# Performance work log

Hardware: AMD Instinct MI355X
Metric: run time of the kernel (lower is better)

The kernel has to match this reference:

```python
import jax, jax.numpy as jnp
import numpy as np

D = 256; H = 4; DK = D // H
MAX_ATOMS = 13; EDGE_NUM = 78; PAD = 799; K = 20
PREFIX = MAX_ATOMS * 2 + 2 + EDGE_NUM * 4   # 340, tokens that get positional encoding
SEQ = PREFIX + K                             # 360
NPAIR = EDGE_NUM + MAX_ATOMS                 # 91 atom pairs (i,j), j up to max_atoms
DFF = 2048; MSP = 800; B = 256

# ---- static pair / gather index tables (numpy, computed once) ----
def _pairs():
    pi, pj, pe = [], [], []
    for i in range(MAX_ATOMS):
        base = sum(MAX_ATOMS - jj - 1 for jj in range(i))  # getEdgeIdx prefix
        for j in range(i + 1, MAX_ATOMS + 1):
            pi.append(i); pj.append(j); pe.append(base + (j - i) - 1)
    return np.array(pi), np.array(pj), np.array(pe)

PI, PJ, PEI = _pairs()
_eb = MAX_ATOMS * 2 + 2 + 2 * PEI           # edge feature start in encoder output (stride 2)
GIDX = np.stack([2*PI, 2*PI+1, 2*PJ, 2*PJ+1, _eb, _eb+1, _eb+2, _eb+3], axis=1)  # (91,8)
ZMASK = np.ones((NPAIR, 8), np.float32)
ZMASK[PJ == MAX_ATOMS, 4:] = 0.0            # j == max_atoms -> edge slots zeroed
ES = (MAX_ATOMS + 1) * 2 + 4 * PEI          # edge slice start in raw src (stride 4)
EIDX = ES[:, None] + np.arange(4)[None, :]  # (91,4)

def _pe_table():
    pe = np.zeros((PREFIX, D), np.float32)
    pos = np.arange(PREFIX, dtype=np.float64)[:, None]
    ev = np.arange(0, D, 2)
    pe[:, ev] = np.sin(pos / 10000.0 ** (2 * ev / D))
    pe[:, ev + 1] = np.cos(pos / 10000.0 ** (2 * (ev + 1) / D))
    return jnp.asarray(pe)

PETAB = _pe_table()

def _norm(x, a, b):
    mu = x.mean(-1, keepdims=True)
    sd = x.std(-1, keepdims=True, ddof=1)   # torch std is unbiased
    return a * (x - mu) / (sd + 1e-6) + b

def _out_mask(src):
    # vectorized get_pad_mask10; later conditions override earlier ones
    ai = src[:, 2*PI + 1]; aj = src[:, 2*PJ + 1]
    ti = src[:, 2*PI];     tj = src[:, 2*PJ]
    c1 = (ai == 2) | (aj == 2)                                  # -> [0,0,1]
    c2 = (tj == 1) | (ai == 1) | (aj == 1)                      # -> [0,1,1]
    c3 = (ti == PAD) | (tj == PAD) | (ai == 0) | (aj == 0)      # -> [1,1,1]
    c4 = jnp.asarray(PJ < MAX_ATOMS)[None, :] & jnp.any(src[:, EIDX] == 1, axis=-1)
    m111 = c3 | c4
    return jnp.stack([m111, m111 | c2, m111 | c2 | c1], axis=-1)  # (B,91,3) bool


def setup_inputs() -> dict:
    key = jax.random.key(0)
    ks = jax.random.split(key, 12)
    g = lambda k, shape, s=0.02: jax.random.normal(k, shape, jnp.float32) * s
    emb = g(ks[0], (MSP, D), 1.0).at[PAD].set(0.0)  # nn.Embedding zeroes padding row
    return {
        'src': jax.random.randint(ks[1], (B, SEQ), 0, MSP, dtype=jnp.int32),
        'emb': emb,
        'wq': g(ks[2], (D, D)), 'bq': jnp.zeros((D,), jnp.float32),
        'wk': g(ks[3], (D, D)), 'bk': jnp.zeros((D,), jnp.float32),
        'wv': g(ks[4], (D, D)), 'bv': jnp.zeros((D,), jnp.float32),
        'wo': g(ks[5], (D, D)), 'bo': jnp.zeros((D,), jnp.float32),
        'n1a': jnp.ones((D,), jnp.float32), 'n1b': jnp.zeros((D,), jnp.float32),
        'n2a': jnp.ones((D,), jnp.float32), 'n2b': jnp.zeros((D,), jnp.float32),
        'w1': g(ks[6], (D, DFF)), 'b1': jnp.zeros((DFF,), jnp.float32),
        'w2': g(ks[7], (DFF, D)), 'b2': jnp.zeros((D,), jnp.float32),
        'wl': g(ks[8], (8 * D, 3)), 'bl': jnp.zeros((3,), jnp.float32),
    }


def reference(src, emb, wq, bq, wk, bk, wv, bv, wo, bo, n1a, n1b, n2a, n2b,
              w1, b1, w2, b2, wl, bl):
    Bn, S = src.shape
    x = emb[src]                                             # (B,S,D)
    # positional encoding (scale + PE) only on first PREFIX tokens, dropout=eval/no-op
    xp = x[:, :PREFIX] * jnp.sqrt(jnp.float32(D)) + PETAB
    x = jnp.concatenate([xp, x[:, PREFIX:]], axis=1)
    pad = src != PAD                                         # (B,S) query-row mask
    # encoder layer (pre-norm, residual)
    x2 = _norm(x, n1a, n1b)
    def heads(w, b):
        return (x2 @ w + b).reshape(Bn, S, H, DK).transpose(0, 2, 1, 3)
    q, kk, v = heads(wq, bq), heads(wk, bk), heads(wv, bv)
    sc = jnp.einsum('bhqd,bhkd->bhqk', q, kk) / jnp.sqrt(jnp.float32(DK))
    sc = jnp.where(pad[:, None, :, None], sc, jnp.float32(-1e9))  # mask broadcasts over keys
    ctx = jnp.einsum('bhqk,bhkd->bhqd', jax.nn.softmax(sc, axis=-1), v)
    x = x + ctx.transpose(0, 2, 1, 3).reshape(Bn, S, D) @ wo + bo
    x2 = _norm(x, n2a, n2b)
    x = x + jax.nn.relu(x2 @ w1 + b1) @ w2 + b2
    # triangular atom-pair gather + concat, vectorized via static index table
    feat = x[:, GIDX] * jnp.asarray(ZMASK)[None, :, :, None]  # (B,91,8,D)
    logits = feat.reshape(Bn, NPAIR, 8 * D) @ wl + bl         # (B,91,3)
    return jnp.where(_out_mask(src), jnp.float32(-1e9), logits)
```

## Files before the change

kernel.cpp:

```cpp
#include <hip/hip_runtime.h>
#include <hip/hip_bf16.h>
#include <math.h>


using bf16 = __hip_bfloat16;
typedef __attribute__((ext_vector_type(4))) float f32x4;
typedef __attribute__((ext_vector_type(16))) float f32x16;
typedef long long i64;
typedef unsigned char uchar;

static __device__ __forceinline__ float wave_sum64(float v){
  #pragma unroll
  for (int o = 32; o >= 1; o >>= 1) v += __shfl_xor(v, o, 64);
  return v;
}

static __device__ __forceinline__ void gl_lds16(const void* g, void* l){
  __builtin_amdgcn_global_load_lds((const __attribute__((address_space(1))) void*)g,
                                   (__attribute__((address_space(3))) void*)l, 16, 0, 0);
}

static __device__ __forceinline__ void barrier_lgkm(){
  asm volatile("s_waitcnt lgkmcnt(0)" ::: "memory");
  __builtin_amdgcn_s_barrier();
}

static __device__ __forceinline__ unsigned pack2(float a, float b){
  union { bf16 h[2]; unsigned u; } u;
  u.h[0] = __float2bfloat16(a); u.h[1] = __float2bfloat16(b);
  return u.u;
}

static __device__ __forceinline__ uchar f2f8(float v){
  return (uchar)(__builtin_amdgcn_cvt_pk_fp8_f32(v, 0.f, 0, false) & 0xff);
}
static __device__ __forceinline__ unsigned pack4_fp8(float a, float b, float c, float d){
  int v = __builtin_amdgcn_cvt_pk_fp8_f32(a, b, 0, false);
  v = __builtin_amdgcn_cvt_pk_fp8_f32(c, d, v, true);
  return (unsigned)v;
}

static __device__ __forceinline__ float fexp2(float x){
  float r;
  asm("v_exp_f32 %0, %1" : "=v"(r) : "v"(x));
  return r;
}

__global__ __launch_bounds__(256) void cvt_all(
    const float* s0, const float* s1, const float* s2, const float* s3,
    const float* s4, const float* s5,
    uchar* d0, uchar* d1, uchar* d2, uchar* d3, uchar* d4, uchar* d5)
{
  __shared__ float t[32][33];
  const float* srcs[6] = {s0, s1, s2, s3, s4, s5};
  uchar* dsts[6] = {d0, d1, d2, d3, d4, d5};
  const int Ks[6] = {256, 256, 256, 256, 256, 2048};
  const int Ns[6] = {256, 256, 256, 256, 2048, 256};
  const int offs[7] = {0, 64, 128, 192, 256, 768, 1280};
  int bid = blockIdx.x, j = 5;
  #pragma unroll
  for (int q = 4; q >= 0; q--) if (bid < offs[q + 1]) j = q;
  int local = bid - offs[j];
  int K = Ks[j], N = Ns[j];
  const float* src = srcs[j];
  uchar* dst = dsts[j];
  int kt = K >> 5;
  int kb = (local % kt) * 32, nb = (local / kt) * 32;
  int tx = threadIdx.x & 31, ty = threadIdx.x >> 5;
  #pragma unroll
  for (int dy = 0; dy < 32; dy += 8)
    t[ty + dy][tx] = src[(size_t)(kb + ty + dy) * N + nb + tx];
  __syncthreads();
  #pragma unroll
  for (int dy = 0; dy < 32; dy += 8)
    dst[(size_t)(nb + ty + dy) * K + kb + tx] = f2f8(t[tx][ty + dy]);
}

__global__ __launch_bounds__(256) void embed_ln1(
    const int* __restrict__ src, const float* __restrict__ emb,
    const float* __restrict__ na, const float* __restrict__ nb,
    bf16* __restrict__ x, uchar* __restrict__ xn8)
{
  int row  = blockIdx.x * 4 + (threadIdx.x >> 6);
  int lane = threadIdx.x & 63;
  int s = row % 360;
  int tok = src[row];
  float4 v = *(const float4*)(emb + (size_t)tok * 256 + lane * 4);
  float vv[4] = {v.x, v.y, v.z, v.w};
  if (s < 340){
    const float C = (-2.0f / 256.0f) * 13.287712379549449f;
    #pragma unroll
    for (int t = 0; t < 4; t++){
      int c = lane * 4 + t;
      float ang = (float)s * exp2f(C * (float)c);
      float pe = (c & 1) ? cosf(ang) : sinf(ang);
      vv[t] = 16.0f * vv[t] + pe;
    }
  }
  float sum = wave_sum64(vv[0] + vv[1] + vv[2] + vv[3]);
  float mu = sum * (1.0f / 256.0f);
  float d0 = vv[0]-mu, d1 = vv[1]-mu, d2 = vv[2]-mu, d3 = vv[3]-mu;
  float sq = wave_sum64(d0*d0 + d1*d1 + d2*d2 + d3*d3);
  float inv = 1.0f / (sqrtf(sq * (1.0f / 255.0f)) + 1e-6f);
  bf16 xo[4] = { __float2bfloat16(vv[0]), __float2bfloat16(vv[1]),
                 __float2bfloat16(vv[2]), __float2bfloat16(vv[3]) };
  *(uint2*)(x + (size_t)row * 256 + lane * 4) = *(uint2*)xo;
  float4 a4 = *(const float4*)(na + lane * 4);
  float4 b4 = *(const float4*)(nb + lane * 4);
  unsigned u = pack4_fp8(a4.x * d0 * inv + b4.x, a4.y * d1 * inv + b4.y,
                         a4.z * d2 * inv + b4.z, a4.w * d3 * inv + b4.w);
  *(unsigned*)(xn8 + (size_t)row * 256 + lane * 4) = u;
}

__global__ __launch_bounds__(256) void ln_k8(
    const bf16* __restrict__ x, const float* __restrict__ na,
    const float* __restrict__ nb, uchar* __restrict__ xn8)
{
  int row  = blockIdx.x * 4 + (threadIdx.x >> 6);
  int lane = threadIdx.x & 63;
  uint2 raw = *(const uint2*)(x + (size_t)row * 256 + lane * 4);
  bf16* xr = (bf16*)&raw;
  float v0 = __bfloat162float(xr[0]), v1 = __bfloat162float(xr[1]);
  float v2 = __bfloat162float(xr[2]), v3 = __bfloat162float(xr[3]);
  float sum = wave_sum64(v0 + v1 + v2 + v3);
  float mu = sum * (1.0f / 256.0f);
  float d0 = v0-mu, d1 = v1-mu, d2 = v2-mu, d3 = v3-mu;
  float sq = wave_sum64(d0*d0 + d1*d1 + d2*d2 + d3*d3);
  float inv = 1.0f / (sqrtf(sq * (1.0f / 255.0f)) + 1e-6f);
  float4 a4 = *(const float4*)(na + lane * 4);
  float4 b4 = *(const float4*)(nb + lane * 4);
  unsigned u = pack4_fp8(a4.x * d0 * inv + b4.x, a4.y * d1 * inv + b4.y,
                         a4.z * d2 * inv + b4.z, a4.w * d3 * inv + b4.w);
  *(unsigned*)(xn8 + (size_t)row * 256 + lane * 4) = u;
}

template<int MODE>
__global__ __launch_bounds__(256) void gemm_k256(
    const uchar* __restrict__ A, const uchar* __restrict__ Bt,
    const float* __restrict__ bias,
    uchar* __restrict__ out8, bf16* __restrict__ xres,
    int N, int nTiles,
    const float* __restrict__ bq, const float* __restrict__ bk)
{
  __shared__ __align__(16) char smem[65536];
  uchar* As = (uchar*)smem;
  uchar* Bs = (uchar*)(smem + 32768);
  uchar* S8 = (uchar*)smem;
  bf16 (*Cs)[136] = (bf16 (*)[136])smem;
  int chunk = gridDim.x >> 3;
  int bi = (blockIdx.x & 7) * chunk + (blockIdx.x >> 3);
  int m0 = (bi / nTiles) * 128, n0 = (bi % nTiles) * 128;
  int tid = threadIdx.x;
  int wave = tid >> 6, lane = tid & 63;
  int wm = (wave >> 1) * 64, wn = (wave & 1) * 64;
  int r32 = lane & 31, half = lane >> 5;

  #pragma unroll
  for (int j = 0; j < 8; j++){
    int c = j * 256 + tid;
    int row = c >> 4, p = c & 15;
    int sl = (p & 8) | ((p & 7) ^ (row & 7));
    gl_lds16(A  + (size_t)(m0 + row) * 256 + sl * 16, As + (size_t)c * 16);
    gl_lds16(Bt + (size_t)(n0 + row) * 256 + sl * 16, Bs + (size_t)c * 16);
  }

  f32x16 acc[2][2];
  #pragma unroll
  for (int mb = 0; mb < 2; mb++)
    #pragma unroll
    for (int nb = 0; nb < 2; nb++)
      #pragma unroll
      for (int e = 0; e < 16; e++) acc[mb][nb][e] = 0.f;

  __syncthreads();

  #pragma unroll
  for (int c = 0; c < 8; c++){
    int l0 = 2 * c + half;
    i64 alo[2], ahi[2], blo[2], bhi[2];
    #pragma unroll
    for (int mb = 0; mb < 2; mb++){
      int row = wm + mb * 32 + r32;
      int st = (l0 & 8) | ((l0 & 7) ^ (row & 7));
      uint4 v = *(const uint4*)(As + row * 256 + st * 16);
      alo[mb] = *(const i64*)&v.x;  ahi[mb] = *(const i64*)&v.z;
    }
    #pragma unroll
    for (int nb = 0; nb < 2; nb++){
      int row = wn + nb * 32 + r32;
      int st = (l0 & 8) | ((l0 & 7) ^ (row & 7));
      uint4 v = *(const uint4*)(Bs + row * 256 + st * 16);
      blo[nb] = *(const i64*)&v.x;  bhi[nb] = *(const i64*)&v.z;
    }
    #pragma unroll
    for (int mb = 0; mb < 2; mb++)
      #pragma unroll
      for (int nb = 0; nb < 2; nb++){
        if (MODE == 5){
          acc[mb][nb] = __builtin_amdgcn_mfma_f32_32x32x16_fp8_fp8(alo[mb], blo[nb], acc[mb][nb], 0, 0, 0);
          acc[mb][nb] = __builtin_amdgcn_mfma_f32_32x32x16_fp8_fp8(ahi[mb], bhi[nb], acc[mb][nb], 0, 0, 0);
        } else {
          acc[mb][nb] = __builtin_amdgcn_mfma_f32_32x32x16_fp8_fp8(blo[nb], alo[mb], acc[mb][nb], 0, 0, 0);
          acc[mb][nb] = __builtin_amdgcn_mfma_f32_32x32x16_fp8_fp8(bhi[nb], ahi[mb], acc[mb][nb], 0, 0, 0);
        }
      }
  }

  __syncthreads();

  if (MODE == 4){
    const int region = n0 >> 8;
    const float* bb = (region == 0 ? bq : bk);
    #pragma unroll
    for (int mb = 0; mb < 2; mb++){
      int m_l = wm + mb * 32 + r32;
      #pragma unroll
      for (int nb = 0; nb < 2; nb++)
        #pragma unroll
        for (int g = 0; g < 4; g++){
          int n_l = wn + nb * 32 + g * 8 + half * 4;
          int bidx = (n0 & 255) + n_l;
          float v0 = acc[mb][nb][g * 4 + 0] + bb[bidx + 0];
          float v1 = acc[mb][nb][g * 4 + 1] + bb[bidx + 1];
          float v2 = acc[mb][nb][g * 4 + 2] + bb[bidx + 2];
          float v3 = acc[mb][nb][g * 4 + 3] + bb[bidx + 3];
          *(unsigned*)(S8 + m_l * 136 + n_l) = pack4_fp8(v0, v1, v2, v3);
        }
    }
    __syncthreads();
    int lr = tid >> 1, seg = tid & 1;
    #pragma unroll
    for (int j = 0; j < 4; j++){
      int nl = seg * 64 + j * 16;
      uint2 a = *(uint2*)(S8 + lr * 136 + nl);
      uint2 b = *(uint2*)(S8 + lr * 136 + nl + 8);
      uint4 st = make_uint4(a.x, a.y, b.x, b.y);
      int m = m0 + lr;
      int b_ = m / 360, s = m - b_ * 360;
      int nnl = (n0 & 255) + nl;
      int h = nnl >> 6, dk = nnl & 63;
      size_t roff = (region == 1) ? 23592960ull : 0ull;
      *(uint4*)(out8 + roff + ((size_t)(b_ * 4 + h) * 360 + s) * 64 + dk) = st;
    }
  } else if (MODE == 5){
    #pragma unroll
    for (int nb = 0; nb < 2; nb++){
      int n_l = wn + nb * 32 + r32;
      float bv_ = bias[n0 + n_l];
      #pragma unroll
      for (int mb = 0; mb < 2; mb++)
        #pragma unroll
        for (int g = 0; g < 4; g++){
          int m_l = wm + mb * 32 + g * 8 + half * 4;
          *(unsigned*)(S8 + n_l * 136 + m_l) =
              pack4_fp8(acc[mb][nb][g * 4 + 0] + bv_, acc[mb][nb][g * 4 + 1] + bv_,
                        acc[mb][nb][g * 4 + 2] + bv_, acc[mb][nb][g * 4 + 3] + bv_);
        }
    }
    __syncthreads();
    int nn = tid >> 1, part = tid & 1;
    int nnl = n0 + nn;
    int h = nnl >> 6, dk = nnl & 63;
    #pragma unroll
    for (int j0 = 0; j0 < 64; j0 += 8){
      int mm = m0 + part * 64 + j0;
      int b_ = mm / 360, s = mm - b_ * 360;
      uint2 val = *(uint2*)(S8 + nn * 136 + part * 64 + j0);
      *(uint2*)(out8 + ((size_t)((b_ * 4 + h) * 64 + dk)) * 360 + s) = val;
    }
  } else {
    #pragma unroll
    for (int hb = 0; hb < 2; hb++){
      if ((wave >> 1) == hb){
        #pragma unroll
        for (int mb = 0; mb < 2; mb++){
          int ml = mb * 32 + r32;
          #pragma unroll
          for (int nb = 0; nb < 2; nb++)
            #pragma unroll
            for (int g = 0; g < 4; g++){
              int nl0 = wn + nb * 32 + g * 8 + half * 4;
              float v0 = acc[mb][nb][g * 4 + 0] + bias[n0 + nl0 + 0];
              float v1 = acc[mb][nb][g * 4 + 1] + bias[n0 + nl0 + 1];
              float v2 = acc[mb][nb][g * 4 + 2] + bias[n0 + nl0 + 2];
              float v3 = acc[mb][nb][g * 4 + 3] + bias[n0 + nl0 + 3];
              *(unsigned*)(&Cs[ml][nl0])     = pack2(v0, v1);
              *(unsigned*)(&Cs[ml][nl0 + 2]) = pack2(v2, v3);
            }
        }
      }
      __syncthreads();
      int mbase = m0 + hb * 64;
      int lr = tid >> 2, seg = tid & 3;
      bf16* op = xres + (size_t)(mbase + lr) * 256 + n0 + seg * 32;
      #pragma unroll
      for (int j = 0; j < 4; j++){
        uint4 cv = *(uint4*)(&Cs[lr][seg * 32 + j * 8]);
        uint4 xv = *(uint4*)(op + j * 8);
        bf16* ca = (bf16*)&cv; bf16* xa = (bf16*)&xv;
        bf16 o8[8];
        #pragma unroll
        for (int t = 0; t < 8; t++)
          o8[t] = __float2bfloat16(__bfloat162float(ca[t]) + __bfloat162float(xa[t]));
        *(uint4*)(op + j * 8) = *(uint4*)o8;
      }
      __syncthreads();
    }
  }
}

__global__ __launch_bounds__(512) void gemm_ffn(
    const uchar* __restrict__ A, const uchar* __restrict__ W1t,
    const uchar* __restrict__ W2t, const float* __restrict__ b1,
    const float* __restrict__ b2, bf16* __restrict__ xres)
{
  extern __shared__ __align__(16) char sm[];
  const int W1OFF = 32768, W2OFF = 98304;
  int bi = (blockIdx.x & 7) * 90 + (blockIdx.x >> 3);
  int m0 = bi * 128;
  int tid = threadIdx.x;
  int wave = tid >> 6, lane = tid & 63;
  int wm = (wave & 1) * 64, wn = (wave >> 1) * 64;
  int wnh = (wave >> 1) * 32;
  int r32 = lane & 31, half = lane >> 5;

  #pragma unroll
  for (int j = 0; j < 4; j++){
    int c = j * 512 + tid;
    int row = c >> 4, p = c & 15;
    int sl = (p & 8) | ((p & 7) ^ (row & 7));
    gl_lds16(A + (size_t)(m0 + row) * 256 + sl * 16, sm + c * 16);
  }
  #pragma unroll
  for (int j = 0; j < 4; j++){
    int c = j * 512 + tid;
    int row1 = c >> 4, p1 = c & 15;
    int sl1 = (p1 & 8) | ((p1 & 7) ^ (row1 & 7));
    gl_lds16(W1t + (size_t)row1 * 256 + sl1 * 16, sm + W1OFF + c * 16);
    int row2 = c >> 3, p2 = c & 7;
    int sl2 = p2 ^ (row2 & 7);
    gl_lds16(W2t + (size_t)row2 * 2048 + sl2 * 16, sm + W2OFF + c * 16);
  }

  f32x16 acc2[2][2];
  #pragma unroll
  for (int mb = 0; mb < 2; mb++)
    #pragma unroll
    for (int nb = 0; nb < 2; nb++)
      #pragma unroll
      for (int e = 0; e < 16; e++) acc2[mb][nb][e] = 0.f;

  __syncthreads();

  i64 Alo[2][8], Ahi[2][8];
  #pragma unroll
  for (int c = 0; c < 8; c++){
    int l0 = 2 * c + half;
    #pragma unroll
    for (int mb = 0; mb < 2; mb++){
      int row = wm + mb * 32 + r32;
      int st = (l0 & 8) | ((l0 & 7) ^ (row & 7));
      uint4 v = *(const uint4*)(sm + row * 256 + st * 16);
      Alo[mb][c] = *(const i64*)&v.x;  Ahi[mb][c] = *(const i64*)&v.z;
    }
  }

  int cur = 0;
  for (int s = 0; s < 16; s++){
    const int w1o = W1OFF + cur * 32768;
    const int w2o = W2OFF + cur * 32768;

    f32x16 acc1[2];
    #pragma unroll
    for (int mb = 0; mb < 2; mb++)
      #pragma unroll
      for (int e = 0; e < 16; e++) acc1[mb][e] = 0.f;
    #pragma unroll
    for (int c = 0; c < 8; c++){
      int l0 = 2 * c + half;
      int roww = wnh + r32;
      int stw = (l0 & 8) | ((l0 & 7) ^ (roww & 7));
      uint4 w = *(const uint4*)(sm + w1o + roww * 256 + stw * 16);
      i64 wlo = *(const i64*)&w.x, whi = *(const i64*)&w.z;
      #pragma unroll
      for (int mb = 0; mb < 2; mb++){
        acc1[mb] = __builtin_amdgcn_mfma_f32_32x32x16_fp8_fp8(wlo, Alo[mb][c], acc1[mb], 0, 0, 0);
        acc1[mb] = __builtin_amdgcn_mfma_f32_32x32x16_fp8_fp8(whi, Ahi[mb][c], acc1[mb], 0, 0, 0);
      }
    }
    barrier_lgkm();

    if (s < 15){
      int nxt = cur ^ 1;
      #pragma unroll
      for (int j = 0; j < 4; j++){
        int c = j * 512 + tid;
        int row1 = c >> 4, p1 = c & 15;
        int sl1 = (p1 & 8) | ((p1 & 7) ^ (row1 & 7));
        gl_lds16(W1t + (size_t)((s + 1) * 128 + row1) * 256 + sl1 * 16,
                 sm + W1OFF + nxt * 32768 + c * 16);
        int row2 = c >> 3, p2 = c & 7;
        int sl2 = p2 ^ (row2 & 7);
        gl_lds16(W2t + (size_t)row2 * 2048 + (s + 1) * 128 + sl2 * 16,
                 sm + W2OFF + nxt * 32768 + c * 16);
      }
    }

    #pragma unroll
    for (int mb = 0; mb < 2; mb++){
      int m = wm + mb * 32 + r32;
      #pragma unroll
      for (int g = 0; g < 4; g++){
        int n_l = wnh + g * 8 + half * 4;
        float4 bv = *(const float4*)(b1 + s * 128 + n_l);
        float v0 = fmaxf(acc1[mb][g * 4 + 0] + bv.x, 0.f);
        float v1 = fmaxf(acc1[mb][g * 4 + 1] + bv.y, 0.f);
        float v2 = fmaxf(acc1[mb][g * 4 + 2] + bv.z, 0.f);
        float v3 = fmaxf(acc1[mb][g * 4 + 3] + bv.w, 0.f);
        int sl = (n_l >> 4) ^ (m & 7);
        *(unsigned*)(sm + w1o + m * 128 + sl * 16 + (n_l & 15)) =
            pack4_fp8(v0, v1, v2, v3);
      }
    }
    barrier_lgkm();

    #pragma unroll
    for (int c = 0; c < 4; c++){
      int l0 = 2 * c + half;
      i64 hlo[2], hhi[2], wlo[2], whi[2];
      #pragma unroll
      for (int mb = 0; mb < 2; mb++){
        int row = wm + mb * 32 + r32;
        int st = l0 ^ (row & 7);
        uint4 v = *(const uint4*)(sm + w1o + row * 128 + st * 16);
        hlo[mb] = *(const i64*)&v.x;  hhi[mb] = *(const i64*)&v.z;
      }
      #pragma unroll
      for (int nb = 0; nb < 2; nb++){
        int row = wn + nb * 32 + r32;
        int st = l0 ^ (row & 7);
        uint4 v = *(const uint4*)(sm + w2o + row * 128 + st * 16);
        wlo[nb] = *(const i64*)&v.x;  whi[nb] = *(const i64*)&v.z;
      }
      #pragma unroll
      for (int mb = 0; mb < 2; mb++)
        #pragma unroll
        for (int nb = 0; nb < 2; nb++){
          acc2[mb][nb] = __builtin_amdgcn_mfma_f32_32x32x16_fp8_fp8(wlo[nb], hlo[mb], acc2[mb][nb], 0, 0, 0);
          acc2[mb][nb] = __builtin_amdgcn_mfma_f32_32x32x16_fp8_fp8(whi[nb], hhi[mb], acc2[mb][nb], 0, 0, 0);
        }
    }
    __syncthreads();
    cur ^= 1;
  }

  bf16 (*Cs)[136] = (bf16 (*)[136])(sm + W1OFF);
  #pragma unroll
  for (int mb = 0; mb < 2; mb++){
    int ml = wm + mb * 32 + r32;
    #pragma unroll
    for (int nb = 0; nb < 2; nb++)
      #pragma unroll
      for (int g = 0; g < 4; g++){
        int nl0 = wn + nb * 32 + g * 8 + half * 4;
        float4 bv = *(const float4*)(b2 + nl0);
        float v0 = acc2[mb][nb][g * 4 + 0] + bv.x;
        float v1 = acc2[mb][nb][g * 4 + 1] + bv.y;
        float v2 = acc2[mb][nb][g * 4 + 2] + bv.z;
        float v3 = acc2[mb][nb][g * 4 + 3] + bv.w;
        *(unsigned*)(&Cs[ml][nl0])     = pack2(v0, v1);
        *(unsigned*)(&Cs[ml][nl0 + 2]) = pack2(v2, v3);
      }
  }
  __syncthreads();
  int lr = tid >> 2, seg = tid & 3;
  bf16* op = xres + (size_t)(m0 + lr) * 256 + seg * 64;
  #pragma unroll
  for (int j = 0; j < 8; j++){
    uint4 cv = *(uint4*)(&Cs[lr][seg * 64 + j * 8]);
    uint4 xv = *(uint4*)(op + j * 8);
    bf16* ca = (bf16*)&cv; bf16* xa = (bf16*)&xv;
    bf16 o8[8];
    #pragma unroll
    for (int t = 0; t < 8; t++)
      o8[t] = __float2bfloat16(__bfloat162float(ca[t]) + __bfloat162float(xa[t]));
    *(uint4*)(op + j * 8) = *(uint4*)o8;
  }
}

template<bool TAIL>
static __device__ __forceinline__ void attn_step(
    int kc, const uchar (*Ks)[80], uchar (*Pb)[16][48],
    const uchar* __restrict__ vb, int wave, int r, int qd,
    const i64* qa0, const i64* qa1, float* lsum, f32x4 (*accO)[4])
{
  int krow0 = kc * 32 + r;
  int krow1 = krow0 + 16;
  if (TAIL){ if (krow0 > 359) krow0 = 359; if (krow1 > 359) krow1 = 359; }
  i64 kf00 = *(const i64*)(&Ks[krow0][qd * 8]);
  i64 kf01 = *(const i64*)(&Ks[krow0][32 + qd * 8]);
  i64 kf10 = *(const i64*)(&Ks[krow1][qd * 8]);
  i64 kf11 = *(const i64*)(&Ks[krow1][32 + qd * 8]);
  i64 vf[4];
  #pragma unroll
  for (int dt = 0; dt < 4; dt++)
    vf[dt] = *(const i64*)(vb + (size_t)(dt * 16 + r) * 360 + kc * 32 + qd * 8);

  const float CEXP = 0.18033688011112042f;

  #pragma unroll
  for (int tl = 0; tl < 3; tl++){
    f32x4 z0 = {0.f, 0.f, 0.f, 0.f}, z1 = {0.f, 0.f, 0.f, 0.f};
    z0 = __builtin_amdgcn_mfma_f32_16x16x32_fp8_fp8(kf00, qa0[tl], z0, 0, 0, 0);
    z0 = __builtin_amdgcn_mfma_f32_16x16x32_fp8_fp8(kf01, qa1[tl], z0, 0, 0, 0);
    z1 = __builtin_amdgcn_mfma_f32_16x16x32_fp8_fp8(kf10, qa0[tl], z1, 0, 0, 0);
    z1 = __builtin_amdgcn_mfma_f32_16x16x32_fp8_fp8(kf11, qa1[tl], z1, 0, 0, 0);
    float p0[4], p1[4];
    #pragma unroll
    for (int i = 0; i < 4; i++){
      p0[i] = fexp2(z0[i] * CEXP);
      p1[i] = fexp2(z1[i] * CEXP);
      if (TAIL){
        if (kc * 32 + qd * 4 + i >= 360) p0[i] = 0.f;
        if (kc * 32 + 16 + qd * 4 + i >= 360) p1[i] = 0.f;
      }
      lsum[tl] += p0[i] + p1[i];
    }
    *(unsigned*)(&Pb[wave][r][qd * 4])      = pack4_fp8(p0[0], p0[1], p0[2], p0[3]);
    *(unsigned*)(&Pb[wave][r][16 + qd * 4]) = pack4_fp8(p1[0], p1[1], p1[2], p1[3]);
    asm volatile("s_waitcnt lgkmcnt(0)" ::: "memory");
    i64 pa = *(const i64*)(&Pb[wave][r][qd * 8]);
    #pragma unroll
    for (int dt = 0; dt < 4; dt++)
      accO[tl][dt] = __builtin_amdgcn_mfma_f32_16x16x32_fp8_fp8(pa, vf[dt], accO[tl][dt], 0, 0, 0);
    asm volatile("s_waitcnt lgkmcnt(0)" ::: "memory");
  }
}

__global__ __launch_bounds__(512) void attn5(
    const uchar* __restrict__ q, const uchar* __restrict__ kk, const uchar* __restrict__ vt,
    const int* __restrict__ src, uchar* __restrict__ ctx8)
{
  __shared__ __align__(16) uchar smem[34944];
  uchar (*Ks)[80]     = (uchar (*)[80])smem;
  uchar (*Pb)[16][48] = (uchar (*)[16][48])(smem + 28800);
  int bh = blockIdx.x;
  int b = bh >> 2, h = bh & 3;
  int wave = threadIdx.x >> 6, lane = threadIdx.x & 63;
  int r = lane & 15, qd = lane >> 4;
  const uchar* qb = q  + (size_t)bh * 360 * 64;
  const uchar* kb = kk + (size_t)bh * 360 * 64;
  const uchar* vb = vt + (size_t)bh * 64 * 360;
  const int* srow = src + b * 360;

  for (int c = threadIdx.x; c < 1440; c += 512){
    int row = c >> 2, g = c & 3;
    *(uint4*)(&Ks[row][g * 16]) = *(const uint4*)(kb + row * 64 + g * 16);
  }
  __syncthreads();

  i64 qa0[3], qa1[3];
  float lsum[3];
  f32x4 accO[3][4];
  #pragma unroll
  for (int tl = 0; tl < 3; tl++){
    int qt = wave * 3 + tl;
    int qg = qt * 16 + r;
    int qrow = qg > 359 ? 359 : qg;
    bool qp = (qg < 360) && (srow[qg] == 799);
    i64 a0 = *(const i64*)(qb + qrow * 64 + qd * 8);
    i64 a1 = *(const i64*)(qb + qrow * 64 + 32 + qd * 8);
    qa0[tl] = qp ? 0 : a0;
    qa1[tl] = qp ? 0 : a1;
    lsum[tl] = 0.f;
    #pragma unroll
    for (int dt = 0; dt < 4; dt++) accO[tl][dt] = (f32x4){0.f, 0.f, 0.f, 0.f};
  }

  for (int kc = 0; kc < 11; kc++)
    attn_step<false>(kc, Ks, Pb, vb, wave, r, qd, qa0, qa1, lsum, accO);
  attn_step<true>(11, Ks, Pb, vb, wave, r, qd, qa0, qa1, lsum, accO);

  __syncthreads();
  uchar* Cw = smem + wave * 1280;

  #pragma unroll
  for (int tl = 0; tl < 3; tl++){
    float ls = lsum[tl];
    ls += __shfl_xor(ls, 16, 64);
    ls += __shfl_xor(ls, 32, 64);
    float invl = 1.0f / ls;
    #pragma unroll
    for (int dt = 0; dt < 4; dt++)
      *(unsigned*)(Cw + r * 80 + dt * 16 + qd * 4) =
          pack4_fp8(accO[tl][dt][0] * invl, accO[tl][dt][1] * invl,
                    accO[tl][dt][2] * invl, accO[tl][dt][3] * invl);
    asm volatile("s_waitcnt lgkmcnt(0)" ::: "memory");
    int qt = wave * 3 + tl;
    int qglob = qt * 16 + r;
    if (qglob < 360)
      *(uint4*)(ctx8 + ((size_t)(b * 360 + qglob)) * 256 + h * 64 + qd * 16) =
          *(uint4*)(Cw + r * 80 + qd * 16);
    asm volatile("s_waitcnt lgkmcnt(0)" ::: "memory");
  }
}

__global__ __launch_bounds__(256) void head_k(
    const bf16* __restrict__ x, const int* __restrict__ src,
    const float* __restrict__ wl, const float* __restrict__ bl,
    float* __restrict__ out)
{
  __shared__ bf16 Xs[192][264];
  int b = blockIdx.x;
  int tid = threadIdx.x;
  int wave = tid >> 6, lane = tid & 63;
  int g = lane >> 3, sub = lane & 7;

  const bf16* xb = x + (size_t)b * 360 * 256;
  for (int it = 0; it < 24; it++){
    int idx = tid + it * 256;
    int row = idx >> 5, col = idx & 31;
    *(uint4*)(&Xs[row][col * 8]) = *(const uint4*)(xb + row * 256 + col * 8);
  }

  float wv[96];
  {
    const float4* wr4 = (const float4*)(wl + (size_t)(g * 256 + sub * 32) * 3);
    #pragma unroll
    for (int c = 0; c < 24; c++) *(float4*)(&wv[c * 4]) = wr4[c];
  }
  float bl0 = bl[0], bl1 = bl[1], bl2 = bl[2];
  const int* sr = src + b * 360;
  __syncthreads();

  for (int p = wave; p < 91; p += 4){
    int i = 0, rem = p;
    while (rem >= 13 - i){ rem -= 13 - i; i++; }
    int j = i + 1 + rem;
    int base = 12 * i - (i * (i - 1)) / 2;
    int pe = base + (j - i) - 1;
    int eb = 28 + 2 * pe;

    int idxg;
    if (g == 0) idxg = 2 * i;
    else if (g == 1) idxg = 2 * i + 1;
    else if (g == 2) idxg = 2 * j;
    else if (g == 3) idxg = 2 * j + 1;
    else idxg = eb + (g - 4);
    bool zm = !(g >= 4 && j == 13);

    uint4 xv[4];
    #pragma unroll
    for (int c = 0; c < 4; c++) xv[c] = *(uint4*)(&Xs[idxg][sub * 32 + c * 8]);
    const bf16* xa = (const bf16*)xv;
    float a0 = 0.f, a1 = 0.f, a2 = 0.f;
    #pragma unroll
    for (int t = 0; t < 32; t++){
      float f = zm ? __bfloat162float(xa[t]) : 0.0f;
      a0 += f * wv[t * 3 + 0];
      a1 += f * wv[t * 3 + 1];
      a2 += f * wv[t * 3 + 2];
    }
    #pragma unroll
    for (int o = 1; o < 64; o <<= 1){
      a0 += __shfl_xor(a0, o, 64);
      a1 += __shfl_xor(a1, o, 64);
      a2 += __shfl_xor(a2, o, 64);
    }
    if (lane == 0){
      int ti = sr[2 * i], ai = sr[2 * i + 1], tj = sr[2 * j], aj = sr[2 * j + 1];
      bool c1 = (ai == 2) || (aj == 2);
      bool c2 = (tj == 1) || (ai == 1) || (aj == 1);
      bool c3 = (ti == 799) || (tj == 799) || (ai == 0) || (aj == 0);
      bool c4 = false;
      if (j < 13){
        int es = 28 + 4 * pe;
        c4 = (sr[es] == 1) || (sr[es + 1] == 1) || (sr[es + 2] == 1) || (sr[es + 3] == 1);
      }
      bool m1 = c3 || c4, m2 = m1 || c2, m3 = m2 || c1;
      float* op = out + ((size_t)b * 91 + p) * 3;
      op[0] = m1 ? -1.0e9f : (a0 + bl0);
      op[1] = m2 ? -1.0e9f : (a1 + bl1);
      op[2] = m3 ? -1.0e9f : (a2 + bl2);
    }
  }
}

extern "C" void kernel_launch(void* const* d_in, const int* in_sizes, int n_in,
                              void* d_out, int out_size, void* d_ws, size_t ws_size,
                              hipStream_t stream)
{
  const int*   src = (const int*)  d_in[0];
  const float* emb = (const float*)d_in[1];
  const float* wq  = (const float*)d_in[2];  const float* bq = (const float*)d_in[3];
  const float* wk  = (const float*)d_in[4];  const float* bk = (const float*)d_in[5];
  const float* wv  = (const float*)d_in[6];  const float* bv = (const float*)d_in[7];
  const float* wo  = (const float*)d_in[8];  const float* bo = (const float*)d_in[9];
  const float* n1a = (const float*)d_in[10]; const float* n1b = (const float*)d_in[11];
  const float* n2a = (const float*)d_in[12]; const float* n2b = (const float*)d_in[13];
  const float* w1  = (const float*)d_in[14]; const float* b1 = (const float*)d_in[15];
  const float* w2  = (const float*)d_in[16]; const float* b2 = (const float*)d_in[17];
  const float* wl  = (const float*)d_in[18]; const float* bl = (const float*)d_in[19];
  float* out = (float*)d_out;

  if (ws_size < 191365120ull) return;

  char* ws = (char*)d_ws;
  bf16*  x    = (bf16*)(ws);
  uchar* xn8  = (uchar*)(ws + 47185920ull);
  char*  R    = ws + 70778880ull;
  uchar* q8   = (uchar*)(R);
  uchar* vt8  = (uchar*)(R + 47185920ull);
  char*  wC   = ws + 165150720ull;
  uchar* wqkv8 = (uchar*)(wC);
  uchar* wo8   = (uchar*)(wC + 196608);
  uchar* w1f8T = (uchar*)(wC + 262144);
  uchar* w2f8T = (uchar*)(wC + 786432);

  cvt_all<<<1280, 256, 0, stream>>>(wq, wk, wv, wo, w1, w2,
                                    wqkv8, wqkv8 + 65536, wqkv8 + 131072,
                                    wo8, w1f8T, w2f8T);

  embed_ln1<<<23040, 256, 0, stream>>>(src, emb, n1a, n1b, x, xn8);

  gemm_k256<4><<<2880, 256, 0, stream>>>(xn8, wqkv8, nullptr, q8, nullptr,
                                         512, 4, bq, bk);
  gemm_k256<5><<<1440, 256, 0, stream>>>(xn8, wqkv8 + 131072, bv, vt8, nullptr,
                                         256, 2, nullptr, nullptr);

  attn5<<<1024, 512, 0, stream>>>(q8, q8 + 23592960ull, vt8, src, xn8 );

  gemm_k256<3><<<1440, 256, 0, stream>>>(xn8, wo8, bo, nullptr, x,
                                         256, 2, nullptr, nullptr);

  ln_k8<<<23040, 256, 0, stream>>>(x, n2a, n2b, xn8);

  gemm_ffn<<<720, 512, 163840, stream>>>(xn8, w1f8T, w2f8T, b1, b2, x);

  head_k<<<256, 256, 0, stream>>>(x, src, wl, bl, out);
}
```

Measured before the change: 498.1 us.

## Widen LDS XOR swizzle to 16 slots, prefetch FFN weights earlier, raise MFMA priority

The LDS swizzle changes from an 8-way XOR inside each 128-byte half-row to a full 16-slot XOR across the 256-byte row. The FFN hidden tile and the W2 tile are repacked as paired rows so they use the same 256-byte swizzled layout. This targets LDS bank conflicts on the wide fragment reads. In the fused FFN loop, the next-stage W1/W2 global-to-LDS prefetch now starts before the first GEMM instead of after its barrier, giving the loads more time to overlap with MFMA work. s_setprio raises wave priority around the MFMA loops, at the cost of more complex address arithmetic.

```diff
diff --git a/kernel.cpp b/kernel.cpp
--- a/kernel.cpp
+++ b/kernel.cpp
@@ -159,7 +159,7 @@
   for (int j = 0; j < 8; j++){
     int c = j * 256 + tid;
     int row = c >> 4, p = c & 15;
-    int sl = (p & 8) | ((p & 7) ^ (row & 7));
+    int sl = p ^ (row & 15);
     gl_lds16(A  + (size_t)(m0 + row) * 256 + sl * 16, As + (size_t)c * 16);
     gl_lds16(Bt + (size_t)(n0 + row) * 256 + sl * 16, Bs + (size_t)c * 16);
   }
@@ -174,6 +174,7 @@
 
   __syncthreads();
 
+  __builtin_amdgcn_s_setprio(1);
   #pragma unroll
   for (int c = 0; c < 8; c++){
     int l0 = 2 * c + half;
@@ -181,14 +182,14 @@
     #pragma unroll
     for (int mb = 0; mb < 2; mb++){
       int row = wm + mb * 32 + r32;
-      int st = (l0 & 8) | ((l0 & 7) ^ (row & 7));
+      int st = l0 ^ (row & 15);
       uint4 v = *(const uint4*)(As + row * 256 + st * 16);
       alo[mb] = *(const i64*)&v.x;  ahi[mb] = *(const i64*)&v.z;
     }
     #pragma unroll
     for (int nb = 0; nb < 2; nb++){
       int row = wn + nb * 32 + r32;
-      int st = (l0 & 8) | ((l0 & 7) ^ (row & 7));
+      int st = l0 ^ (row & 15);
       uint4 v = *(const uint4*)(Bs + row * 256 + st * 16);
       blo[nb] = *(const i64*)&v.x;  bhi[nb] = *(const i64*)&v.z;
     }
@@ -205,6 +206,7 @@
         }
       }
   }
+  __builtin_amdgcn_s_setprio(0);
 
   __syncthreads();
 
@@ -328,18 +330,20 @@
   for (int j = 0; j < 4; j++){
     int c = j * 512 + tid;
     int row = c >> 4, p = c & 15;
-    int sl = (p & 8) | ((p & 7) ^ (row & 7));
+    int sl = p ^ (row & 15);
     gl_lds16(A + (size_t)(m0 + row) * 256 + sl * 16, sm + c * 16);
   }
   #pragma unroll
   for (int j = 0; j < 4; j++){
     int c = j * 512 + tid;
     int row1 = c >> 4, p1 = c & 15;
-    int sl1 = (p1 & 8) | ((p1 & 7) ^ (row1 & 7));
+    int sl1 = p1 ^ (row1 & 15);
     gl_lds16(W1t + (size_t)row1 * 256 + sl1 * 16, sm + W1OFF + c * 16);
-    int row2 = c >> 3, p2 = c & 7;
-    int sl2 = p2 ^ (row2 & 7);
-    gl_lds16(W2t + (size_t)row2 * 2048 + sl2 * 16, sm + W2OFF + c * 16);
+    int sr = c >> 4, sl = c & 15;
+    int v = sl ^ (sr & 15);
+    int p3 = v >> 1, rp = v & 1;
+    int row2 = sr * 2 + rp;
+    gl_lds16(W2t + (size_t)row2 * 2048 + p3 * 16, sm + W2OFF + c * 16);
   }
 
   f32x16 acc2[2][2];
@@ -359,7 +363,7 @@
     #pragma unroll
     for (int mb = 0; mb < 2; mb++){
       int row = wm + mb * 32 + r32;
-      int st = (l0 & 8) | ((l0 & 7) ^ (row & 7));
+      int st = l0 ^ (row & 15);
       uint4 v = *(const uint4*)(sm + row * 256 + st * 16);
       Alo[mb][c] = *(const i64*)&v.x;  Ahi[mb][c] = *(const i64*)&v.z;
     }
@@ -370,16 +374,35 @@
     const int w1o = W1OFF + cur * 32768;
     const int w2o = W2OFF + cur * 32768;
 
+    if (s < 15){
+      int nxt = cur ^ 1;
+      #pragma unroll
+      for (int j = 0; j < 4; j++){
+        int c = j * 512 + tid;
+        int row1 = c >> 4, p1 = c & 15;
+        int sl1 = p1 ^ (row1 & 15);
+        gl_lds16(W1t + (size_t)((s + 1) * 128 + row1) * 256 + sl1 * 16,
+                 sm + W1OFF + nxt * 32768 + c * 16);
+        int sr = c >> 4, sl = c & 15;
+        int v = sl ^ (sr & 15);
+        int p3 = v >> 1, rp = v & 1;
+        int row2 = sr * 2 + rp;
+        gl_lds16(W2t + (size_t)row2 * 2048 + (s + 1) * 128 + p3 * 16,
+                 sm + W2OFF + nxt * 32768 + c * 16);
+      }
+    }
+
     f32x16 acc1[2];
     #pragma unroll
     for (int mb = 0; mb < 2; mb++)
       #pragma unroll
       for (int e = 0; e < 16; e++) acc1[mb][e] = 0.f;
+    __builtin_amdgcn_s_setprio(1);
     #pragma unroll
     for (int c = 0; c < 8; c++){
       int l0 = 2 * c + half;
       int roww = wnh + r32;
-      int stw = (l0 & 8) | ((l0 & 7) ^ (roww & 7));
+      int stw = l0 ^ (roww & 15);
       uint4 w = *(const uint4*)(sm + w1o + roww * 256 + stw * 16);
       i64 wlo = *(const i64*)&w.x, whi = *(const i64*)&w.z;
       #pragma unroll
@@ -388,27 +411,13 @@
         acc1[mb] = __builtin_amdgcn_mfma_f32_32x32x16_fp8_fp8(whi, Ahi[mb][c], acc1[mb], 0, 0, 0);
       }
     }
+    __builtin_amdgcn_s_setprio(0);
     barrier_lgkm();
-
-    if (s < 15){
-      int nxt = cur ^ 1;
-      #pragma unroll
-      for (int j = 0; j < 4; j++){
-        int c = j * 512 + tid;
-        int row1 = c >> 4, p1 = c & 15;
-        int sl1 = (p1 & 8) | ((p1 & 7) ^ (row1 & 7));
-        gl_lds16(W1t + (size_t)((s + 1) * 128 + row1) * 256 + sl1 * 16,
-                 sm + W1OFF + nxt * 32768 + c * 16);
-        int row2 = c >> 3, p2 = c & 7;
-        int sl2 = p2 ^ (row2 & 7);
-        gl_lds16(W2t + (size_t)row2 * 2048 + (s + 1) * 128 + sl2 * 16,
-                 sm + W2OFF + nxt * 32768 + c * 16);
-      }
-    }
 
     #pragma unroll
     for (int mb = 0; mb < 2; mb++){
       int m = wm + mb * 32 + r32;
+      int sr = m >> 1;
       #pragma unroll
       for (int g = 0; g < 4; g++){
         int n_l = wnh + g * 8 + half * 4;
@@ -417,13 +426,14 @@
         float v1 = fmaxf(acc1[mb][g * 4 + 1] + bv.y, 0.f);
         float v2 = fmaxf(acc1[mb][g * 4 + 2] + bv.z, 0.f);
         float v3 = fmaxf(acc1[mb][g * 4 + 3] + bv.w, 0.f);
-        int sl = (n_l >> 4) ^ (m & 7);
-        *(unsigned*)(sm + w1o + m * 128 + sl * 16 + (n_l & 15)) =
+        int slot = (((n_l >> 4) << 1) | (m & 1)) ^ (sr & 15);
+        *(unsigned*)(sm + w1o + sr * 256 + slot * 16 + (n_l & 15)) =
             pack4_fp8(v0, v1, v2, v3);
       }
     }
     barrier_lgkm();
 
+    __builtin_amdgcn_s_setprio(1);
     #pragma unroll
     for (int c = 0; c < 4; c++){
       int l0 = 2 * c + half;
@@ -431,15 +441,17 @@
       #pragma unroll
       for (int mb = 0; mb < 2; mb++){
         int row = wm + mb * 32 + r32;
-        int st = l0 ^ (row & 7);
-        uint4 v = *(const uint4*)(sm + w1o + row * 128 + st * 16);
+        int sr = row >> 1;
+        int slot = ((l0 << 1) | (row & 1)) ^ (sr & 15);
+        uint4 v = *(const uint4*)(sm + w1o + sr * 256 + slot * 16);
         hlo[mb] = *(const i64*)&v.x;  hhi[mb] = *(const i64*)&v.z;
       }
       #pragma unroll
       for (int nb = 0; nb < 2; nb++){
         int row = wn + nb * 32 + r32;
-        int st = l0 ^ (row & 7);
-        uint4 v = *(const uint4*)(sm + w2o + row * 128 + st * 16);
+        int sr = row >> 1;
+        int slot = ((l0 << 1) | (row & 1)) ^ (sr & 15);
+        uint4 v = *(const uint4*)(sm + w2o + sr * 256 + slot * 16);
         wlo[nb] = *(const i64*)&v.x;  whi[nb] = *(const i64*)&v.z;
       }
       #pragma unroll
@@ -450,6 +462,7 @@
           acc2[mb][nb] = __builtin_amdgcn_mfma_f32_32x32x16_fp8_fp8(whi[nb], hhi[mb], acc2[mb][nb], 0, 0, 0);
         }
     }
+    __builtin_amdgcn_s_setprio(0);
     __syncthreads();
     cur ^= 1;
   }
```

Result: slower. 516.1 us (+3.6%).

## Halve FFN tile rows and drop LDS double buffering to fit two blocks per CU

Applied to the files above, without the earlier changes.

The fused FFN kernel moves from 128-row tiles with 512 threads and double-buffered weight tiles (160 KB LDS) to 64-row tiles with 256 threads and one weight buffer (80 KB LDS), launched as 1440 blocks. The aim is to let two blocks share a CU, so one block's loads overlap the other's compute instead of relying on prefetch inside a block. In exchange, each block now waits on its own weight loads every step with an extra barrier. W1/W2 are also fetched twice as often overall, which puts more pressure on L2.

```diff
diff --git a/kernel.cpp b/kernel.cpp
--- a/kernel.cpp
+++ b/kernel.cpp
@@ -309,31 +309,31 @@
   }
 }
 
-__global__ __launch_bounds__(512) void gemm_ffn(
+__global__ __launch_bounds__(256) void gemm_ffn(
     const uchar* __restrict__ A, const uchar* __restrict__ W1t,
     const uchar* __restrict__ W2t, const float* __restrict__ b1,
     const float* __restrict__ b2, bf16* __restrict__ xres)
 {
   extern __shared__ __align__(16) char sm[];
-  const int W1OFF = 32768, W2OFF = 98304;
-  int bi = (blockIdx.x & 7) * 90 + (blockIdx.x >> 3);
-  int m0 = bi * 128;
+  const int W1OFF = 16384, W2OFF = 49152;
+  int bi = (blockIdx.x & 7) * 180 + (blockIdx.x >> 3);
+  int m0 = bi * 64;
   int tid = threadIdx.x;
   int wave = tid >> 6, lane = tid & 63;
-  int wm = (wave & 1) * 64, wn = (wave >> 1) * 64;
-  int wnh = (wave >> 1) * 32;
+  int wn  = wave * 64;
+  int wnh = wave * 32;
   int r32 = lane & 31, half = lane >> 5;
 
   #pragma unroll
   for (int j = 0; j < 4; j++){
-    int c = j * 512 + tid;
+    int c = j * 256 + tid;
     int row = c >> 4, p = c & 15;
     int sl = (p & 8) | ((p & 7) ^ (row & 7));
     gl_lds16(A + (size_t)(m0 + row) * 256 + sl * 16, sm + c * 16);
   }
   #pragma unroll
-  for (int j = 0; j < 4; j++){
-    int c = j * 512 + tid;
+  for (int j = 0; j < 8; j++){
+    int c = j * 256 + tid;
     int row1 = c >> 4, p1 = c & 15;
     int sl1 = (p1 & 8) | ((p1 & 7) ^ (row1 & 7));
     gl_lds16(W1t + (size_t)row1 * 256 + sl1 * 16, sm + W1OFF + c * 16);
@@ -358,18 +358,14 @@
     int l0 = 2 * c + half;
     #pragma unroll
     for (int mb = 0; mb < 2; mb++){
-      int row = wm + mb * 32 + r32;
+      int row = mb * 32 + r32;
       int st = (l0 & 8) | ((l0 & 7) ^ (row & 7));
       uint4 v = *(const uint4*)(sm + row * 256 + st * 16);
       Alo[mb][c] = *(const i64*)&v.x;  Ahi[mb][c] = *(const i64*)&v.z;
     }
   }
 
-  int cur = 0;
   for (int s = 0; s < 16; s++){
-    const int w1o = W1OFF + cur * 32768;
-    const int w2o = W2OFF + cur * 32768;
-
     f32x16 acc1[2];
     #pragma unroll
     for (int mb = 0; mb < 2; mb++)
@@ -380,7 +376,7 @@
       int l0 = 2 * c + half;
       int roww = wnh + r32;
       int stw = (l0 & 8) | ((l0 & 7) ^ (roww & 7));
-      uint4 w = *(const uint4*)(sm + w1o + roww * 256 + stw * 16);
+      uint4 w = *(const uint4*)(sm + W1OFF + roww * 256 + stw * 16);
       i64 wlo = *(const i64*)&w.x, whi = *(const i64*)&w.z;
       #pragma unroll
       for (int mb = 0; mb < 2; mb++){
@@ -390,25 +386,9 @@
     }
     barrier_lgkm();
 
-    if (s < 15){
-      int nxt = cur ^ 1;
-      #pragma unroll
-      for (int j = 0; j < 4; j++){
-        int c = j * 512 + tid;
-        int row1 = c >> 4, p1 = c & 15;
-        int sl1 = (p1 & 8) | ((p1 & 7) ^ (row1 & 7));
-        gl_lds16(W1t + (size_t)((s + 1) * 128 + row1) * 256 + sl1 * 16,
-                 sm + W1OFF + nxt * 32768 + c * 16);
-        int row2 = c >> 3, p2 = c & 7;
-        int sl2 = p2 ^ (row2 & 7);
-        gl_lds16(W2t + (size_t)row2 * 2048 + (s + 1) * 128 + sl2 * 16,
-                 sm + W2OFF + nxt * 32768 + c * 16);
-      }
-    }
-
     #pragma unroll
     for (int mb = 0; mb < 2; mb++){
-      int m = wm + mb * 32 + r32;
+      int m = mb * 32 + r32;
       #pragma unroll
       for (int g = 0; g < 4; g++){
         int n_l = wnh + g * 8 + half * 4;
@@ -418,7 +398,7 @@
         float v2 = fmaxf(acc1[mb][g * 4 + 2] + bv.z, 0.f);
         float v3 = fmaxf(acc1[mb][g * 4 + 3] + bv.w, 0.f);
         int sl = (n_l >> 4) ^ (m & 7);
-        *(unsigned*)(sm + w1o + m * 128 + sl * 16 + (n_l & 15)) =
+        *(unsigned*)(sm + W1OFF + m * 128 + sl * 16 + (n_l & 15)) =
             pack4_fp8(v0, v1, v2, v3);
       }
     }
@@ -430,16 +410,16 @@
       i64 hlo[2], hhi[2], wlo[2], whi[2];
       #pragma unroll
       for (int mb = 0; mb < 2; mb++){
-        int row = wm + mb * 32 + r32;
+        int row = mb * 32 + r32;
         int st = l0 ^ (row & 7);
-        uint4 v = *(const uint4*)(sm + w1o + row * 128 + st * 16);
+        uint4 v = *(const uint4*)(sm + W1OFF + row * 128 + st * 16);
         hlo[mb] = *(const i64*)&v.x;  hhi[mb] = *(const i64*)&v.z;
       }
       #pragma unroll
       for (int nb = 0; nb < 2; nb++){
         int row = wn + nb * 32 + r32;
         int st = l0 ^ (row & 7);
-        uint4 v = *(const uint4*)(sm + w2o + row * 128 + st * 16);
+        uint4 v = *(const uint4*)(sm + W2OFF + row * 128 + st * 16);
         wlo[nb] = *(const i64*)&v.x;  whi[nb] = *(const i64*)&v.z;
       }
       #pragma unroll
@@ -450,14 +430,29 @@
           acc2[mb][nb] = __builtin_amdgcn_mfma_f32_32x32x16_fp8_fp8(whi[nb], hhi[mb], acc2[mb][nb], 0, 0, 0);
         }
     }
-    __syncthreads();
-    cur ^= 1;
-  }
-
-  bf16 (*Cs)[136] = (bf16 (*)[136])(sm + W1OFF);
+    barrier_lgkm();
+
+    if (s < 15){
+      #pragma unroll
+      for (int j = 0; j < 8; j++){
+        int c = j * 256 + tid;
+        int row1 = c >> 4, p1 = c & 15;
+        int sl1 = (p1 & 8) | ((p1 & 7) ^ (row1 & 7));
+        gl_lds16(W1t + (size_t)((s + 1) * 128 + row1) * 256 + sl1 * 16,
+                 sm + W1OFF + c * 16);
+        int row2 = c >> 3, p2 = c & 7;
+        int sl2 = p2 ^ (row2 & 7);
+        gl_lds16(W2t + (size_t)row2 * 2048 + (s + 1) * 128 + sl2 * 16,
+                 sm + W2OFF + c * 16);
+      }
+      __syncthreads();
+    }
+  }
+
+  bf16 (*Cs)[264] = (bf16 (*)[264])(sm + W1OFF);
   #pragma unroll
   for (int mb = 0; mb < 2; mb++){
-    int ml = wm + mb * 32 + r32;
+    int ml = mb * 32 + r32;
     #pragma unroll
     for (int nb = 0; nb < 2; nb++)
       #pragma unroll
@@ -472,7 +467,7 @@
         *(unsigned*)(&Cs[ml][nl0 + 2]) = pack2(v2, v3);
       }
   }
-  __syncthreads();
+  barrier_lgkm();
   int lr = tid >> 2, seg = tid & 3;
   bf16* op = xres + (size_t)(m0 + lr) * 256 + seg * 64;
   #pragma unroll
@@ -735,7 +730,7 @@
 
   ln_k8<<<23040, 256, 0, stream>>>(x, n2a, n2b, xn8);
 
-  gemm_ffn<<<720, 512, 163840, stream>>>(xn8, w1f8T, w2f8T, b1, b2, x);
+  gemm_ffn<<<1440, 256, 81920, stream>>>(xn8, w1f8T, w2f8T, b1, b2, x);
 
   head_k<<<256, 256, 0, stream>>>(x, src, wl, bl, out);
 }
```

Result: slower. 550.7 us (+10.6%).
